# Kernel optimization log

Hardware: AMD Instinct MI355X
Metric: run time of the kernel (lower is better)

Reference implementation:

```python
import jax, jax.numpy as jnp
import numpy as np

N_NODES = 50000
E_EDGES = 800000
NODE_DIM = 64
HID = 128


def _leaky(x):
    return jnp.where(x > 0, x, 0.2 * x)


def _gat_conv(x, W, a_src, a_dst, b, src, dst, heads, out_ch, concat):
    # x: [N, in]; W: [in, heads*out]; a_src/a_dst: [heads, out]
    N = x.shape[0]
    h = (x @ W).reshape(N, heads, out_ch)            # [N, H, C]
    s = (h * a_src[None]).sum(-1)                    # [N, H]
    d = (h * a_dst[None]).sum(-1)                    # [N, H]
    e = _leaky(s[src] + d[dst])                      # [E, H]
    m = jax.ops.segment_max(e, dst, num_segments=N)  # segment softmax (stable)
    ex = jnp.exp(e - m[dst])
    denom = jax.ops.segment_sum(ex, dst, num_segments=N)
    alpha = ex / denom[dst]                          # [E, H] (self-loops -> denom>0)
    out = jax.ops.segment_sum(h[src] * alpha[..., None], dst, num_segments=N)
    out = out.reshape(N, heads * out_ch) if concat else out.mean(axis=1)
    return out + b


def setup_inputs() -> dict:
    key = jax.random.key(0)
    ks = jax.random.split(key, 16)
    sc = 0.1
    inp = {
        "x": jax.random.normal(ks[0], (N_NODES, NODE_DIM), jnp.float32),
        "edge_index": jax.random.randint(ks[1], (2, E_EDGES), 0, N_NODES, jnp.int64),
        "fc_w": jax.random.normal(ks[2], (NODE_DIM, HID), jnp.float32) * sc,
        "fc_b": jnp.zeros((HID,), jnp.float32),
        "W1": jax.random.normal(ks[3], (HID, 2 * HID), jnp.float32) * sc,
        "asrc1": jax.random.normal(ks[4], (2, HID), jnp.float32) * sc,
        "adst1": jax.random.normal(ks[5], (2, HID), jnp.float32) * sc,
        "b1": jnp.zeros((2 * HID,), jnp.float32),
        "Wm": jax.random.normal(ks[6], (4, 2 * HID, 2 * HID), jnp.float32) * sc,
        "asrcm": jax.random.normal(ks[7], (4, 2, HID), jnp.float32) * sc,
        "adstm": jax.random.normal(ks[8], (4, 2, HID), jnp.float32) * sc,
        "bm": jnp.zeros((4, 2 * HID), jnp.float32),
        "W6": jax.random.normal(ks[9], (2 * HID, HID), jnp.float32) * sc,
        "asrc6": jax.random.normal(ks[10], (1, HID), jnp.float32) * sc,
        "adst6": jax.random.normal(ks[11], (1, HID), jnp.float32) * sc,
        "b6": jnp.zeros((HID,), jnp.float32),
    }
    return inp


def reference(x, edge_index, fc_w, fc_b, W1, asrc1, adst1, b1,
              Wm, asrcm, adstm, bm, W6, asrc6, adst6, b6):
    N = x.shape[0]
    loops = jnp.arange(N, dtype=edge_index.dtype)
    src = jnp.concatenate([edge_index[0], loops])  # add_self_loops=True (PyG default)
    dst = jnp.concatenate([edge_index[1], loops])

    out = jax.nn.relu(x @ fc_w + fc_b)
    out = _gat_conv(out, W1, asrc1, adst1, b1, src, dst, 2, HID, True)
    for i in range(4):
        out = _gat_conv(out, Wm[i], asrcm[i], adstm[i], bm[i], src, dst, 2, HID, True)
    out = _gat_conv(out, W6, asrc6, adst6, b6, src, dst, 1, HID, True)
    return out
```

## Files before the change

kernel.cpp:

```cpp
#include <hip/hip_runtime.h>
#include <cstdint>
#include <cstddef>

#define NN 50000
#define EE 800000
#define ET 850000

typedef unsigned short ushort_t;
typedef unsigned int uint_t;
using frag_ab = __attribute__((ext_vector_type(8))) short;
using f32x4   = __attribute__((ext_vector_type(4))) float;

__device__ inline ushort_t f2b(float x) {
  union { float f; unsigned int u; } c; c.f = x;
  unsigned int u = c.u;
  u += 0x7fffu + ((u >> 16) & 1u);
  return (ushort_t)(u >> 16);
}
__device__ inline float b2f(uint_t u) {
  union { unsigned int u; float f; } c; c.u = u << 16;
  return c.f;
}

__device__ inline void gload16(const ushort_t* g, ushort_t* l) {
  __builtin_amdgcn_global_load_lds(
      (const __attribute__((address_space(1))) unsigned int*)g,
      (__attribute__((address_space(3))) unsigned int*)l, 16, 0, 0);
}

__global__ __launch_bounds__(256) void k_count(const int* __restrict__ edge,
                                               int* __restrict__ counts) {
  int e = blockIdx.x * 256 + threadIdx.x;
  if (e >= ET) return;
  int dd = (e < EE) ? edge[EE + e] : (e - EE);
  atomicAdd(&counts[dd], 1);
}

__global__ __launch_bounds__(1024) void k_scan1(const int* __restrict__ counts,
                                                int* __restrict__ scn,
                                                int* __restrict__ bsum) {
  __shared__ int tmp[1024];
  int tid = threadIdx.x;
  int idx = blockIdx.x * 1024 + tid;
  int v = (idx < NN) ? counts[idx] : 0;
  tmp[tid] = v;
  __syncthreads();
  for (int o = 1; o < 1024; o <<= 1) {
    int u = (tid >= o) ? tmp[tid - o] : 0;
    __syncthreads();
    tmp[tid] += u;
    __syncthreads();
  }
  if (idx < NN) scn[idx] = tmp[tid] - v;
  if (tid == 1023) bsum[blockIdx.x] = tmp[1023];
}

__global__ __launch_bounds__(64) void k_scan2(const int* __restrict__ bsum,
                                              int* __restrict__ boff) {
  int l = threadIdx.x;
  const int NB = (NN + 1023) / 1024;
  int v = (l < NB) ? bsum[l] : 0;
  int own = v;
  for (int o = 1; o < 64; o <<= 1) {
    int u = __shfl_up(v, o);
    if (l >= o) v += u;
  }
  if (l < NB) boff[l] = v - own;
}

__global__ __launch_bounds__(1024) void k_scan3(const int* __restrict__ scn,
                                                const int* __restrict__ boff,
                                                int* __restrict__ row_ptr,
                                                int* __restrict__ cursor) {
  int idx = blockIdx.x * 1024 + threadIdx.x;
  if (idx < NN) {
    int v = scn[idx] + boff[blockIdx.x];
    row_ptr[idx] = v;
    cursor[idx] = v;
  }
  if (idx == 0) row_ptr[NN] = ET;
}

__global__ __launch_bounds__(256) void k_fill(const int* __restrict__ edge,
                                              int* __restrict__ cursor,
                                              int* __restrict__ col_src) {
  int e = blockIdx.x * 256 + threadIdx.x;
  if (e >= ET) return;
  int ss, dd;
  if (e < EE) { ss = edge[e]; dd = edge[EE + e]; }
  else        { ss = dd = e - EE; }
  int pos = atomicAdd(&cursor[dd], 1);
  col_src[pos] = ss;
}

__global__ __launch_bounds__(256) void k_prep_w(const float* __restrict__ fc_w,
                                                const float* __restrict__ W1,
                                                const float* __restrict__ Wm,
                                                const float* __restrict__ W6,
                                                ushort_t* __restrict__ fcWt,
                                                ushort_t* __restrict__ W1t,
                                                ushort_t* __restrict__ Wmt,
                                                ushort_t* __restrict__ W6t) {
  int i = blockIdx.x * 256 + threadIdx.x;
  if (i < 128 * 64) { int n = i >> 6, k = i & 63; fcWt[i] = f2b(fc_w[k * 128 + n]); return; }
  i -= 128 * 64;
  if (i < 256 * 128) { int n = i >> 7, k = i & 127; W1t[i] = f2b(W1[k * 256 + n]); return; }
  i -= 256 * 128;
  if (i < 4 * 256 * 256) {
    int l = i >> 16, r2 = i & 65535, n = r2 >> 8, k = r2 & 255;
    Wmt[i] = f2b(Wm[(size_t)l * 65536 + k * 256 + n]); return;
  }
  i -= 4 * 256 * 256;
  if (i < 128 * 256) { int n = i >> 8, k = i & 255; W6t[i] = f2b(W6[k * 128 + n]); return; }
}

__global__ __launch_bounds__(256) void k_gemm_f32(const float* __restrict__ A,
                                                  const ushort_t* __restrict__ Bt,
                                                  ushort_t* __restrict__ C,
                                                  int M, int K, int Nc,
                                                  const float* __restrict__ bias) {
  __shared__ ushort_t As[128 * 40];
  __shared__ ushort_t Bs[128 * 40];
  int row0 = blockIdx.x * 128;
  int col0 = blockIdx.y * 128;
  int t = threadIdx.x;
  int lane = t & 63, w = t >> 6;
  int wr = w >> 1, wc = w & 1;
  int r = lane & 15, kg = lane >> 4;

  f32x4 acc[4][4];
#pragma unroll
  for (int m = 0; m < 4; ++m)
#pragma unroll
    for (int n = 0; n < 4; ++n) acc[m][n] = (f32x4){0.f, 0.f, 0.f, 0.f};

  for (int k0 = 0; k0 < K; k0 += 32) {
    __syncthreads();
#pragma unroll
    for (int rep = 0; rep < 4; ++rep) {
      int c = t + rep * 256;
      int row = c >> 3, kc = c & 7;
      int grow = row0 + row;
      if (grow < M) {
        float4 v = *(const float4*)&A[(size_t)grow * K + k0 + kc * 4];
        ushort4 u;
        u.x = f2b(v.x); u.y = f2b(v.y); u.z = f2b(v.z); u.w = f2b(v.w);
        *(ushort4*)&As[row * 40 + kc * 4] = u;
      }
    }
#pragma unroll
    for (int rep = 0; rep < 2; ++rep) {
      int c = t + rep * 256;
      int row = c >> 2, kc = c & 3;
      uint4 v = *(const uint4*)&Bt[(size_t)(col0 + row) * K + k0 + kc * 8];
      *(uint4*)&Bs[row * 40 + kc * 8] = v;
    }
    __syncthreads();

    frag_ab a[4], b[4];
#pragma unroll
    for (int m = 0; m < 4; ++m)
      a[m] = *(const frag_ab*)&As[(wr * 64 + m * 16 + r) * 40 + kg * 8];
#pragma unroll
    for (int n = 0; n < 4; ++n)
      b[n] = *(const frag_ab*)&Bs[(wc * 64 + n * 16 + r) * 40 + kg * 8];
#pragma unroll
    for (int m = 0; m < 4; ++m)
#pragma unroll
      for (int n = 0; n < 4; ++n)
        acc[m][n] = __builtin_amdgcn_mfma_f32_16x16x32_bf16(a[m], b[n], acc[m][n], 0, 0, 0);
  }

#pragma unroll
  for (int m = 0; m < 4; ++m) {
    int gr0 = row0 + wr * 64 + m * 16 + kg * 4;
#pragma unroll
    for (int q = 0; q < 4; ++q) {
      int grow = gr0 + q;
      if (grow >= M) continue;
#pragma unroll
      for (int n = 0; n < 4; ++n) {
        int gcol = col0 + wc * 64 + n * 16 + r;
        float val = acc[m][n][q] + bias[gcol];
        val = fmaxf(val, 0.f);
        C[(size_t)grow * Nc + gcol] = f2b(val);
      }
    }
  }
}

__global__ __launch_bounds__(256) void k_gemm64(const ushort_t* __restrict__ A,
                                                const ushort_t* __restrict__ Bt,
                                                ushort_t* __restrict__ C,
                                                int M, int K, int Nc,
                                                const float* __restrict__ a_src,
                                                const float* __restrict__ a_dst,
                                                float* __restrict__ sbuf,
                                                float* __restrict__ dbuf,
                                                int H) {
  __shared__ ushort_t As[128 * 64];
  __shared__ ushort_t Bs[128 * 64];
  __shared__ float sdred[128][2][2];
  int row0 = blockIdx.x * 128;
  int col0 = blockIdx.y * 128;
  int t = threadIdx.x;
  int lane = t & 63, w = t >> 6;
  int wr = w >> 1, wc = w & 1;
  int r = lane & 15, kg = lane >> 4;

  f32x4 acc[4][4];
#pragma unroll
  for (int m = 0; m < 4; ++m)
#pragma unroll
    for (int n = 0; n < 4; ++n) acc[m][n] = (f32x4){0.f, 0.f, 0.f, 0.f};

  for (int k0 = 0; k0 < K; k0 += 64) {
    __syncthreads();
#pragma unroll
    for (int i = 0; i < 4; ++i) {
      int c = w * 4 + i;
      int b = c * 1024 + lane * 16;
      int row = b >> 7;
      int ks = ((b >> 4) & 7) ^ (row & 7);
      const ushort_t* ga = A + (size_t)(row0 + row) * K + k0 + ks * 8;
      if (row0 + row < M) gload16(ga, &As[c * 512]);
      const ushort_t* gb = Bt + (size_t)(col0 + row) * K + k0 + ks * 8;
      gload16(gb, &Bs[c * 512]);
    }
    __syncthreads();

#pragma unroll
    for (int kk = 0; kk < 2; ++kk) {
      frag_ab af[4], bf[4];
#pragma unroll
      for (int m = 0; m < 4; ++m) {
        int row = wr * 64 + m * 16 + r;
        int byte = row * 128 + ((kk * 64 + kg * 16) ^ ((row & 7) << 4));
        af[m] = *(const frag_ab*)((const char*)As + byte);
      }
#pragma unroll
      for (int n = 0; n < 4; ++n) {
        int row = wc * 64 + n * 16 + r;
        int byte = row * 128 + ((kk * 64 + kg * 16) ^ ((row & 7) << 4));
        bf[n] = *(const frag_ab*)((const char*)Bs + byte);
      }
#pragma unroll
      for (int m = 0; m < 4; ++m)
#pragma unroll
        for (int n = 0; n < 4; ++n)
          acc[m][n] = __builtin_amdgcn_mfma_f32_16x16x32_bf16(af[m], bf[n], acc[m][n], 0, 0, 0);
    }
  }

  int head = blockIdx.y;
  float as_[4], ad_[4];
#pragma unroll
  for (int n = 0; n < 4; ++n) {
    int cloc = wc * 64 + n * 16 + r;
    as_[n] = a_src[head * 128 + cloc];
    ad_[n] = a_dst[head * 128 + cloc];
  }

#pragma unroll
  for (int m = 0; m < 4; ++m) {
    int gr0 = row0 + wr * 64 + m * 16 + kg * 4;
#pragma unroll
    for (int q = 0; q < 4; ++q) {
      int grow = gr0 + q;
      float ps = 0.f, pd = 0.f;
      if (grow < M) {
#pragma unroll
        for (int n = 0; n < 4; ++n) {
          int gcol = col0 + wc * 64 + n * 16 + r;
          float val = acc[m][n][q];
          ps += val * as_[n]; pd += val * ad_[n];
          C[(size_t)grow * Nc + gcol] = f2b(val);
        }
      }
#pragma unroll
      for (int o = 1; o < 16; o <<= 1) {
        ps += __shfl_xor(ps, o);
        pd += __shfl_xor(pd, o);
      }
      int row_loc = wr * 64 + m * 16 + kg * 4 + q;
      if (r == 0) { sdred[row_loc][wc][0] = ps; sdred[row_loc][wc][1] = pd; }
    }
  }
  __syncthreads();
  int row = t >> 1, which = t & 1;
  int grow = row0 + row;
  if (grow < M) {
    float v = sdred[row][0][which] + sdred[row][1][which];
    float* dst = which ? dbuf : sbuf;
    dst[(size_t)grow * H + head] = v;
  }
}

__global__ __launch_bounds__(256) void k_agg2(const ushort_t* __restrict__ h2,
                                              const float* __restrict__ s,
                                              const float* __restrict__ dv,
                                              const int* __restrict__ row_ptr,
                                              const int* __restrict__ col_src,
                                              const float* __restrict__ bias,
                                              uint4* __restrict__ out) {
  int wid = threadIdx.x >> 6, l = threadIdx.x & 63;
  int n = blockIdx.x * 4 + wid;
  if (n >= NN) return;
  int beg = row_ptr[n], end = row_ptr[n + 1];
  float2 tdn = ((const float2*)dv)[n];
  float dn0 = tdn.x, dn1 = tdn.y;

  float m0 = -1e30f, d0 = 0.f, m1 = -1e30f, d1 = 0.f;
  for (int e = beg + l; e < end; e += 64) {
    int src = col_src[e];
    float2 sv = ((const float2*)s)[src];
    float x0 = sv.x + dn0; x0 = x0 > 0.f ? x0 : 0.2f * x0;
    if (x0 > m0) { d0 = d0 * __expf(m0 - x0) + 1.f; m0 = x0; } else d0 += __expf(x0 - m0);
    float x1 = sv.y + dn1; x1 = x1 > 0.f ? x1 : 0.2f * x1;
    if (x1 > m1) { d1 = d1 * __expf(m1 - x1) + 1.f; m1 = x1; } else d1 += __expf(x1 - m1);
  }
#pragma unroll
  for (int o = 1; o < 64; o <<= 1) {
    float mo = __shfl_xor(m0, o), dno = __shfl_xor(d0, o);
    float M2 = fmaxf(m0, mo);
    d0 = d0 * __expf(m0 - M2) + dno * __expf(mo - M2);
    m0 = M2;
    mo = __shfl_xor(m1, o); dno = __shfl_xor(d1, o);
    M2 = fmaxf(m1, mo);
    d1 = d1 * __expf(m1 - M2) + dno * __expf(mo - M2);
    m1 = M2;
  }

  int hw = l >> 5, lh = l & 31;
  int hd = lh >> 4;
  const uint4* hrow = (const uint4*)h2;
  float a0 = 0.f, a1 = 0.f, a2 = 0.f, a3 = 0.f;
  float a4 = 0.f, a5 = 0.f, a6 = 0.f, a7 = 0.f;

  for (int c = beg; c < end; c += 32) {
    int cnt = min(32, end - c);
    float alpv = 0.f; int srcv = 0;
    if (l < 2 * cnt) {
      int e = c + (l >> 1), hi = l & 1;
      srcv = col_src[e];
      float x = s[srcv * 2 + hi] + (hi ? dn1 : dn0);
      x = x > 0.f ? x : 0.2f * x;
      alpv = __expf(x - (hi ? m1 : m0));
    }
    int e = 0;
    for (; e + 4 <= cnt + 1; e += 4) {
      int ep0 = e + hw, ep1 = e + 2 + hw;
      int s0 = __shfl(srcv, 2 * ep0);
      int s1 = __shfl(srcv, 2 * ep1);
      float p0 = __shfl(alpv, 2 * ep0 + hd);
      float p1 = __shfl(alpv, 2 * ep1 + hd);
      if (ep0 >= cnt) p0 = 0.f;
      if (ep1 >= cnt) p1 = 0.f;
      uint4 v0 = hrow[(size_t)s0 * 32 + lh];
      uint4 v1 = hrow[(size_t)s1 * 32 + lh];
      a0 = fmaf(p0, b2f(v0.x & 0xffffu), a0); a1 = fmaf(p0, b2f(v0.x >> 16), a1);
      a2 = fmaf(p0, b2f(v0.y & 0xffffu), a2); a3 = fmaf(p0, b2f(v0.y >> 16), a3);
      a4 = fmaf(p0, b2f(v0.z & 0xffffu), a4); a5 = fmaf(p0, b2f(v0.z >> 16), a5);
      a6 = fmaf(p0, b2f(v0.w & 0xffffu), a6); a7 = fmaf(p0, b2f(v0.w >> 16), a7);
      a0 = fmaf(p1, b2f(v1.x & 0xffffu), a0); a1 = fmaf(p1, b2f(v1.x >> 16), a1);
      a2 = fmaf(p1, b2f(v1.y & 0xffffu), a2); a3 = fmaf(p1, b2f(v1.y >> 16), a3);
      a4 = fmaf(p1, b2f(v1.z & 0xffffu), a4); a5 = fmaf(p1, b2f(v1.z >> 16), a5);
      a6 = fmaf(p1, b2f(v1.w & 0xffffu), a6); a7 = fmaf(p1, b2f(v1.w >> 16), a7);
    }
    for (; e < cnt; e += 2) {
      int ep = e + hw;
      int s0 = __shfl(srcv, 2 * ep);
      float p = __shfl(alpv, 2 * ep + hd);
      if (ep >= cnt) p = 0.f;
      uint4 v = hrow[(size_t)s0 * 32 + lh];
      a0 = fmaf(p, b2f(v.x & 0xffffu), a0); a1 = fmaf(p, b2f(v.x >> 16), a1);
      a2 = fmaf(p, b2f(v.y & 0xffffu), a2); a3 = fmaf(p, b2f(v.y >> 16), a3);
      a4 = fmaf(p, b2f(v.z & 0xffffu), a4); a5 = fmaf(p, b2f(v.z >> 16), a5);
      a6 = fmaf(p, b2f(v.w & 0xffffu), a6); a7 = fmaf(p, b2f(v.w >> 16), a7);
    }
  }
  a0 += __shfl_xor(a0, 32); a1 += __shfl_xor(a1, 32);
  a2 += __shfl_xor(a2, 32); a3 += __shfl_xor(a3, 32);
  a4 += __shfl_xor(a4, 32); a5 += __shfl_xor(a5, 32);
  a6 += __shfl_xor(a6, 32); a7 += __shfl_xor(a7, 32);

  if (hw == 0) {
    float dh = hd ? d1 : d0;
    float inv = 1.f / dh;
    float4 b0 = ((const float4*)bias)[2 * lh];
    float4 b1 = ((const float4*)bias)[2 * lh + 1];
    uint4 ov;
    ov.x = (uint_t)f2b(a0 * inv + b0.x) | ((uint_t)f2b(a1 * inv + b0.y) << 16);
    ov.y = (uint_t)f2b(a2 * inv + b0.z) | ((uint_t)f2b(a3 * inv + b0.w) << 16);
    ov.z = (uint_t)f2b(a4 * inv + b1.x) | ((uint_t)f2b(a5 * inv + b1.y) << 16);
    ov.w = (uint_t)f2b(a6 * inv + b1.z) | ((uint_t)f2b(a7 * inv + b1.w) << 16);
    out[(size_t)n * 32 + lh] = ov;
  }
}

__global__ __launch_bounds__(256) void k_agg1(const ushort_t* __restrict__ h2,
                                              const float* __restrict__ s,
                                              const float* __restrict__ dv,
                                              const int* __restrict__ row_ptr,
                                              const int* __restrict__ col_src,
                                              const float* __restrict__ bias,
                                              float* __restrict__ out) {
  int wid = threadIdx.x >> 6, l = threadIdx.x & 63;
  int n = blockIdx.x * 4 + wid;
  if (n >= NN) return;
  int beg = row_ptr[n], end = row_ptr[n + 1];
  float dn0 = dv[n];

  float m0 = -1e30f, d0 = 0.f;
  for (int e = beg + l; e < end; e += 64) {
    float x0 = s[col_src[e]] + dn0;
    x0 = x0 > 0.f ? x0 : 0.2f * x0;
    if (x0 > m0) { d0 = d0 * __expf(m0 - x0) + 1.f; m0 = x0; } else d0 += __expf(x0 - m0);
  }
#pragma unroll
  for (int o = 1; o < 64; o <<= 1) {
    float mo = __shfl_xor(m0, o), dno = __shfl_xor(d0, o);
    float M2 = fmaxf(m0, mo);
    d0 = d0 * __expf(m0 - M2) + dno * __expf(mo - M2);
    m0 = M2;
  }

  int hw = l >> 4, lh = l & 15;
  const uint4* hrow = (const uint4*)h2;
  float a0 = 0.f, a1 = 0.f, a2 = 0.f, a3 = 0.f;
  float a4 = 0.f, a5 = 0.f, a6 = 0.f, a7 = 0.f;

  for (int c = beg; c < end; c += 64) {
    int cnt = min(64, end - c);
    float alpv = 0.f; int srcv = 0;
    if (l < cnt) {
      srcv = col_src[c + l];
      float x = s[srcv] + dn0;
      x = x > 0.f ? x : 0.2f * x;
      alpv = __expf(x - m0);
    }
    for (int e = 0; e < cnt; e += 4) {
      int ep = e + hw;
      int s0 = __shfl(srcv, ep);
      float p = __shfl(alpv, ep);
      if (ep >= cnt) p = 0.f;
      uint4 v = hrow[(size_t)s0 * 16 + lh];
      a0 = fmaf(p, b2f(v.x & 0xffffu), a0); a1 = fmaf(p, b2f(v.x >> 16), a1);
      a2 = fmaf(p, b2f(v.y & 0xffffu), a2); a3 = fmaf(p, b2f(v.y >> 16), a3);
      a4 = fmaf(p, b2f(v.z & 0xffffu), a4); a5 = fmaf(p, b2f(v.z >> 16), a5);
      a6 = fmaf(p, b2f(v.w & 0xffffu), a6); a7 = fmaf(p, b2f(v.w >> 16), a7);
    }
  }
#pragma unroll
  for (int o = 16; o < 64; o <<= 1) {
    a0 += __shfl_xor(a0, o); a1 += __shfl_xor(a1, o);
    a2 += __shfl_xor(a2, o); a3 += __shfl_xor(a3, o);
    a4 += __shfl_xor(a4, o); a5 += __shfl_xor(a5, o);
    a6 += __shfl_xor(a6, o); a7 += __shfl_xor(a7, o);
  }
  if (hw == 0) {
    float inv = 1.f / d0;
    float4 b0 = ((const float4*)bias)[2 * lh];
    float4 b1 = ((const float4*)bias)[2 * lh + 1];
    float4 o0 = make_float4(a0 * inv + b0.x, a1 * inv + b0.y, a2 * inv + b0.z, a3 * inv + b0.w);
    float4 o1 = make_float4(a4 * inv + b1.x, a5 * inv + b1.y, a6 * inv + b1.z, a7 * inv + b1.w);
    ((float4*)out)[(size_t)n * 32 + 2 * lh] = o0;
    ((float4*)out)[(size_t)n * 32 + 2 * lh + 1] = o1;
  }
}

extern "C" void kernel_launch(void* const* d_in, const int* in_sizes, int n_in,
                              void* d_out, int out_size, void* d_ws, size_t ws_size,
                              hipStream_t stream) {
  const float* x     = (const float*)d_in[0];
  const int*   edge  = (const int*)d_in[1];
  const float* fc_w  = (const float*)d_in[2];
  const float* fc_b  = (const float*)d_in[3];
  const float* W1    = (const float*)d_in[4];
  const float* asrc1 = (const float*)d_in[5];
  const float* adst1 = (const float*)d_in[6];
  const float* b1    = (const float*)d_in[7];
  const float* Wm    = (const float*)d_in[8];
  const float* asrcm = (const float*)d_in[9];
  const float* adstm = (const float*)d_in[10];
  const float* bm    = (const float*)d_in[11];
  const float* W6    = (const float*)d_in[12];
  const float* asrc6 = (const float*)d_in[13];
  const float* adst6 = (const float*)d_in[14];
  const float* b6    = (const float*)d_in[15];

  char* w = (char*)d_ws;
  size_t off = 0;
  auto carve = [&](size_t bytes) -> char* {
    char* p = w + off;
    off = (off + bytes + 255) & ~(size_t)255;
    return p;
  };
  ushort_t* feat0 = (ushort_t*)carve((size_t)NN * 256 * 2);
  ushort_t* feat1 = (ushort_t*)carve((size_t)NN * 256 * 2);
  ushort_t* hbuf  = (ushort_t*)carve((size_t)NN * 256 * 2);
  float* sbuf   = (float*)carve((size_t)NN * 2 * 4);
  float* dbuf   = (float*)carve((size_t)NN * 2 * 4);
  ushort_t* fcWt = (ushort_t*)carve((size_t)128 * 64 * 2);
  ushort_t* W1t  = (ushort_t*)carve((size_t)256 * 128 * 2);
  ushort_t* Wmt  = (ushort_t*)carve((size_t)4 * 256 * 256 * 2);
  ushort_t* W6t  = (ushort_t*)carve((size_t)128 * 256 * 2);
  int* counts   = (int*)carve((size_t)NN * 4);
  int* row_ptr  = (int*)carve((size_t)(NN + 1) * 4);
  int* cursor   = (int*)carve((size_t)NN * 4);
  int* col_src  = (int*)carve((size_t)ET * 4);
  int* scn      = (int*)carve((size_t)NN * 4);
  int* bsum     = (int*)carve((size_t)64 * 4);
  int* boff     = (int*)carve((size_t)64 * 4);
  (void)ws_size;

  k_prep_w<<<(335872 + 255) / 256, 256, 0, stream>>>(fc_w, W1, Wm, W6, fcWt, W1t, Wmt, W6t);

  hipMemsetAsync(counts, 0, (size_t)NN * 4, stream);
  int eb = (ET + 255) / 256;
  const int NB = (NN + 1023) / 1024;
  k_count<<<eb, 256, 0, stream>>>(edge, counts);
  k_scan1<<<NB, 1024, 0, stream>>>(counts, scn, bsum);
  k_scan2<<<1, 64, 0, stream>>>(bsum, boff);
  k_scan3<<<NB, 1024, 0, stream>>>(scn, boff, row_ptr, cursor);
  k_fill<<<eb, 256, 0, stream>>>(edge, cursor, col_src);

  dim3 g1((NN + 127) / 128, 1), g2((NN + 127) / 128, 2);
  int ab = (NN + 3) / 4;

  auto gat = [&](const ushort_t* in, int K, const ushort_t* Wt, const float* a_s,
                 const float* a_d, const float* bias, void* outp, int H) {
    k_gemm64<<<(H == 2 ? g2 : g1), 256, 0, stream>>>(
        in, Wt, hbuf, NN, K, H * 128, a_s, a_d, sbuf, dbuf, H);
    if (H == 2)
      k_agg2<<<ab, 256, 0, stream>>>(hbuf, sbuf, dbuf, row_ptr, col_src, bias, (uint4*)outp);
    else
      k_agg1<<<ab, 256, 0, stream>>>(hbuf, sbuf, dbuf, row_ptr, col_src, bias, (float*)outp);
  };

  k_gemm_f32<<<g1, 256, 0, stream>>>(x, fcWt, feat0, NN, 64, 128, fc_b);

  gat(feat0, 128, W1t, asrc1, adst1, b1, feat1, 2);

  const ushort_t* cur = feat1;
  ushort_t* nxt = feat0;
  for (int i = 0; i < 4; ++i) {
    gat(cur, 256, Wmt + (size_t)i * 256 * 256, asrcm + (size_t)i * 2 * 128,
        adstm + (size_t)i * 2 * 128, bm + (size_t)i * 256, nxt, 2);
    const ushort_t* tmp = cur;
    cur = nxt;
    nxt = (ushort_t*)tmp;
  }

  gat(cur, 256, W6t, asrc6, adst6, b6, d_out, 1);
}
```

Before: 599.3 us.

## Add single-pass low-degree path and packed FMA to GAT aggregation kernels

Both aggregation kernels gain a fast path for nodes with degree at most 64. In that path each lane loads its edge's source and score once, and plain max and sum wave reductions replace the online-softmax loop and the second reload of col_src and s. The accumulation now uses packed two-wide FMA on unpacked bf16 pairs with precomputed byte offsets and a fixed unrolled inner loop. Padding lanes carry zero probability instead of a per-edge bound check, and the general path is kept for high-degree nodes.

```diff
diff --git a/kernel.cpp b/kernel.cpp
--- a/kernel.cpp
+++ b/kernel.cpp
@@ -10,6 +10,7 @@
 typedef unsigned int uint_t;
 using frag_ab = __attribute__((ext_vector_type(8))) short;
 using f32x4   = __attribute__((ext_vector_type(4))) float;
+using f32x2   = __attribute__((ext_vector_type(2))) float;
 
 __device__ inline ushort_t f2b(float x) {
   union { float f; unsigned int u; } c; c.f = x;
@@ -20,6 +21,11 @@
 __device__ inline float b2f(uint_t u) {
   union { unsigned int u; float f; } c; c.u = u << 16;
   return c.f;
+}
+__device__ inline f32x2 unp2(uint_t u) {
+  union { uint_t u; float f; } lo, hi;
+  lo.u = u << 16; hi.u = u & 0xffff0000u;
+  f32x2 r; r.x = lo.f; r.y = hi.f; return r;
 }
 
 __device__ inline void gload16(const ushort_t* g, ushort_t* l) {
@@ -307,82 +313,109 @@
   int n = blockIdx.x * 4 + wid;
   if (n >= NN) return;
   int beg = row_ptr[n], end = row_ptr[n + 1];
+  int deg = end - beg;
   float2 tdn = ((const float2*)dv)[n];
   float dn0 = tdn.x, dn1 = tdn.y;
-
-  float m0 = -1e30f, d0 = 0.f, m1 = -1e30f, d1 = 0.f;
-  for (int e = beg + l; e < end; e += 64) {
-    int src = col_src[e];
-    float2 sv = ((const float2*)s)[src];
-    float x0 = sv.x + dn0; x0 = x0 > 0.f ? x0 : 0.2f * x0;
-    if (x0 > m0) { d0 = d0 * __expf(m0 - x0) + 1.f; m0 = x0; } else d0 += __expf(x0 - m0);
-    float x1 = sv.y + dn1; x1 = x1 > 0.f ? x1 : 0.2f * x1;
-    if (x1 > m1) { d1 = d1 * __expf(m1 - x1) + 1.f; m1 = x1; } else d1 += __expf(x1 - m1);
-  }
-#pragma unroll
-  for (int o = 1; o < 64; o <<= 1) {
-    float mo = __shfl_xor(m0, o), dno = __shfl_xor(d0, o);
-    float M2 = fmaxf(m0, mo);
-    d0 = d0 * __expf(m0 - M2) + dno * __expf(mo - M2);
-    m0 = M2;
-    mo = __shfl_xor(m1, o); dno = __shfl_xor(d1, o);
-    M2 = fmaxf(m1, mo);
-    d1 = d1 * __expf(m1 - M2) + dno * __expf(mo - M2);
-    m1 = M2;
-  }
-
-  int hw = l >> 5, lh = l & 31;
-  int hd = lh >> 4;
-  const uint4* hrow = (const uint4*)h2;
-  float a0 = 0.f, a1 = 0.f, a2 = 0.f, a3 = 0.f;
-  float a4 = 0.f, a5 = 0.f, a6 = 0.f, a7 = 0.f;
-
-  for (int c = beg; c < end; c += 32) {
-    int cnt = min(32, end - c);
-    float alpv = 0.f; int srcv = 0;
-    if (l < 2 * cnt) {
-      int e = c + (l >> 1), hi = l & 1;
-      srcv = col_src[e];
-      float x = s[srcv * 2 + hi] + (hi ? dn1 : dn0);
-      x = x > 0.f ? x : 0.2f * x;
-      alpv = __expf(x - (hi ? m1 : m0));
-    }
-    int e = 0;
-    for (; e + 4 <= cnt + 1; e += 4) {
-      int ep0 = e + hw, ep1 = e + 2 + hw;
-      int s0 = __shfl(srcv, 2 * ep0);
-      int s1 = __shfl(srcv, 2 * ep1);
-      float p0 = __shfl(alpv, 2 * ep0 + hd);
-      float p1 = __shfl(alpv, 2 * ep1 + hd);
-      if (ep0 >= cnt) p0 = 0.f;
-      if (ep1 >= cnt) p1 = 0.f;
-      uint4 v0 = hrow[(size_t)s0 * 32 + lh];
-      uint4 v1 = hrow[(size_t)s1 * 32 + lh];
-      a0 = fmaf(p0, b2f(v0.x & 0xffffu), a0); a1 = fmaf(p0, b2f(v0.x >> 16), a1);
-      a2 = fmaf(p0, b2f(v0.y & 0xffffu), a2); a3 = fmaf(p0, b2f(v0.y >> 16), a3);
-      a4 = fmaf(p0, b2f(v0.z & 0xffffu), a4); a5 = fmaf(p0, b2f(v0.z >> 16), a5);
-      a6 = fmaf(p0, b2f(v0.w & 0xffffu), a6); a7 = fmaf(p0, b2f(v0.w >> 16), a7);
-      a0 = fmaf(p1, b2f(v1.x & 0xffffu), a0); a1 = fmaf(p1, b2f(v1.x >> 16), a1);
-      a2 = fmaf(p1, b2f(v1.y & 0xffffu), a2); a3 = fmaf(p1, b2f(v1.y >> 16), a3);
-      a4 = fmaf(p1, b2f(v1.z & 0xffffu), a4); a5 = fmaf(p1, b2f(v1.z >> 16), a5);
-      a6 = fmaf(p1, b2f(v1.w & 0xffffu), a6); a7 = fmaf(p1, b2f(v1.w >> 16), a7);
-    }
-    for (; e < cnt; e += 2) {
-      int ep = e + hw;
-      int s0 = __shfl(srcv, 2 * ep);
-      float p = __shfl(alpv, 2 * ep + hd);
-      if (ep >= cnt) p = 0.f;
-      uint4 v = hrow[(size_t)s0 * 32 + lh];
-      a0 = fmaf(p, b2f(v.x & 0xffffu), a0); a1 = fmaf(p, b2f(v.x >> 16), a1);
-      a2 = fmaf(p, b2f(v.y & 0xffffu), a2); a3 = fmaf(p, b2f(v.y >> 16), a3);
-      a4 = fmaf(p, b2f(v.z & 0xffffu), a4); a5 = fmaf(p, b2f(v.z >> 16), a5);
-      a6 = fmaf(p, b2f(v.w & 0xffffu), a6); a7 = fmaf(p, b2f(v.w >> 16), a7);
-    }
-  }
-  a0 += __shfl_xor(a0, 32); a1 += __shfl_xor(a1, 32);
-  a2 += __shfl_xor(a2, 32); a3 += __shfl_xor(a3, 32);
-  a4 += __shfl_xor(a4, 32); a5 += __shfl_xor(a5, 32);
-  a6 += __shfl_xor(a6, 32); a7 += __shfl_xor(a7, 32);
+  int hw = l >> 5, lh = l & 31, hd = lh >> 4;
+  const char* hb = (const char*)h2 + lh * 16;
+
+  f32x2 A0 = {0.f, 0.f}, A1 = {0.f, 0.f}, A2 = {0.f, 0.f}, A3 = {0.f, 0.f};
+  float d0, d1;
+
+  if (deg <= 64) {
+    int srcv = 0; float x0 = -1e30f, x1 = -1e30f;
+    if (l < deg) {
+      srcv = col_src[beg + l];
+      float2 sv = ((const float2*)s)[srcv];
+      x0 = sv.x + dn0; x0 = x0 > 0.f ? x0 : 0.2f * x0;
+      x1 = sv.y + dn1; x1 = x1 > 0.f ? x1 : 0.2f * x1;
+    }
+    float m0 = x0, m1 = x1;
+#pragma unroll
+    for (int o = 1; o < 64; o <<= 1) {
+      m0 = fmaxf(m0, __shfl_xor(m0, o));
+      m1 = fmaxf(m1, __shfl_xor(m1, o));
+    }
+    float p0 = __expf(x0 - m0), p1 = __expf(x1 - m1);
+    d0 = p0; d1 = p1;
+#pragma unroll
+    for (int o = 1; o < 64; o <<= 1) {
+      d0 += __shfl_xor(d0, o);
+      d1 += __shfl_xor(d1, o);
+    }
+    int offv = srcv << 9;
+    for (int e = 0; e < deg; e += 8) {
+#pragma unroll
+      for (int i = 0; i < 4; ++i) {
+        int ep = e + 2 * i + hw;
+        int off = __shfl(offv, ep);
+        float pa0 = __shfl(p0, ep);
+        float pa1 = __shfl(p1, ep);
+        float pa = hd ? pa1 : pa0;
+        uint4 v = *(const uint4*)(hb + off);
+        f32x2 pp = {pa, pa};
+        A0 = __builtin_elementwise_fma(unp2(v.x), pp, A0);
+        A1 = __builtin_elementwise_fma(unp2(v.y), pp, A1);
+        A2 = __builtin_elementwise_fma(unp2(v.z), pp, A2);
+        A3 = __builtin_elementwise_fma(unp2(v.w), pp, A3);
+      }
+    }
+  } else {
+    float m0 = -1e30f, m1 = -1e30f;
+    d0 = 0.f; d1 = 0.f;
+    for (int e = beg + l; e < end; e += 64) {
+      int src = col_src[e];
+      float2 sv = ((const float2*)s)[src];
+      float x0 = sv.x + dn0; x0 = x0 > 0.f ? x0 : 0.2f * x0;
+      if (x0 > m0) { d0 = d0 * __expf(m0 - x0) + 1.f; m0 = x0; } else d0 += __expf(x0 - m0);
+      float x1 = sv.y + dn1; x1 = x1 > 0.f ? x1 : 0.2f * x1;
+      if (x1 > m1) { d1 = d1 * __expf(m1 - x1) + 1.f; m1 = x1; } else d1 += __expf(x1 - m1);
+    }
+#pragma unroll
+    for (int o = 1; o < 64; o <<= 1) {
+      float mo = __shfl_xor(m0, o), dno = __shfl_xor(d0, o);
+      float M2 = fmaxf(m0, mo);
+      d0 = d0 * __expf(m0 - M2) + dno * __expf(mo - M2);
+      m0 = M2;
+      mo = __shfl_xor(m1, o); dno = __shfl_xor(d1, o);
+      M2 = fmaxf(m1, mo);
+      d1 = d1 * __expf(m1 - M2) + dno * __expf(mo - M2);
+      m1 = M2;
+    }
+    for (int c = beg; c < end; c += 64) {
+      int cnt = min(64, end - c);
+      int srcv = 0; float x0 = -1e30f, x1 = -1e30f;
+      if (l < cnt) {
+        srcv = col_src[c + l];
+        float2 sv = ((const float2*)s)[srcv];
+        x0 = sv.x + dn0; x0 = x0 > 0.f ? x0 : 0.2f * x0;
+        x1 = sv.y + dn1; x1 = x1 > 0.f ? x1 : 0.2f * x1;
+      }
+      float p0 = __expf(x0 - m0), p1 = __expf(x1 - m1);
+      int offv = srcv << 9;
+      for (int e = 0; e < cnt; e += 8) {
+#pragma unroll
+        for (int i = 0; i < 4; ++i) {
+          int ep = e + 2 * i + hw;
+          int off = __shfl(offv, ep);
+          float pa0 = __shfl(p0, ep);
+          float pa1 = __shfl(p1, ep);
+          float pa = hd ? pa1 : pa0;
+          uint4 v = *(const uint4*)(hb + off);
+          f32x2 pp = {pa, pa};
+          A0 = __builtin_elementwise_fma(unp2(v.x), pp, A0);
+          A1 = __builtin_elementwise_fma(unp2(v.y), pp, A1);
+          A2 = __builtin_elementwise_fma(unp2(v.z), pp, A2);
+          A3 = __builtin_elementwise_fma(unp2(v.w), pp, A3);
+        }
+      }
+    }
+  }
+
+  A0.x += __shfl_xor(A0.x, 32); A0.y += __shfl_xor(A0.y, 32);
+  A1.x += __shfl_xor(A1.x, 32); A1.y += __shfl_xor(A1.y, 32);
+  A2.x += __shfl_xor(A2.x, 32); A2.y += __shfl_xor(A2.y, 32);
+  A3.x += __shfl_xor(A3.x, 32); A3.y += __shfl_xor(A3.y, 32);
 
   if (hw == 0) {
     float dh = hd ? d1 : d0;
@@ -390,10 +423,10 @@
     float4 b0 = ((const float4*)bias)[2 * lh];
     float4 b1 = ((const float4*)bias)[2 * lh + 1];
     uint4 ov;
-    ov.x = (uint_t)f2b(a0 * inv + b0.x) | ((uint_t)f2b(a1 * inv + b0.y) << 16);
-    ov.y = (uint_t)f2b(a2 * inv + b0.z) | ((uint_t)f2b(a3 * inv + b0.w) << 16);
-    ov.z = (uint_t)f2b(a4 * inv + b1.x) | ((uint_t)f2b(a5 * inv + b1.y) << 16);
-    ov.w = (uint_t)f2b(a6 * inv + b1.z) | ((uint_t)f2b(a7 * inv + b1.w) << 16);
+    ov.x = (uint_t)f2b(A0.x * inv + b0.x) | ((uint_t)f2b(A0.y * inv + b0.y) << 16);
+    ov.y = (uint_t)f2b(A1.x * inv + b0.z) | ((uint_t)f2b(A1.y * inv + b0.w) << 16);
+    ov.z = (uint_t)f2b(A2.x * inv + b1.x) | ((uint_t)f2b(A2.y * inv + b1.y) << 16);
+    ov.w = (uint_t)f2b(A3.x * inv + b1.z) | ((uint_t)f2b(A3.y * inv + b1.w) << 16);
     out[(size_t)n * 32 + lh] = ov;
   }
 }
@@ -409,61 +442,98 @@
   int n = blockIdx.x * 4 + wid;
   if (n >= NN) return;
   int beg = row_ptr[n], end = row_ptr[n + 1];
+  int deg = end - beg;
   float dn0 = dv[n];
-
-  float m0 = -1e30f, d0 = 0.f;
-  for (int e = beg + l; e < end; e += 64) {
-    float x0 = s[col_src[e]] + dn0;
-    x0 = x0 > 0.f ? x0 : 0.2f * x0;
-    if (x0 > m0) { d0 = d0 * __expf(m0 - x0) + 1.f; m0 = x0; } else d0 += __expf(x0 - m0);
-  }
-#pragma unroll
-  for (int o = 1; o < 64; o <<= 1) {
-    float mo = __shfl_xor(m0, o), dno = __shfl_xor(d0, o);
-    float M2 = fmaxf(m0, mo);
-    d0 = d0 * __expf(m0 - M2) + dno * __expf(mo - M2);
-    m0 = M2;
-  }
-
   int hw = l >> 4, lh = l & 15;
-  const uint4* hrow = (const uint4*)h2;
-  float a0 = 0.f, a1 = 0.f, a2 = 0.f, a3 = 0.f;
-  float a4 = 0.f, a5 = 0.f, a6 = 0.f, a7 = 0.f;
-
-  for (int c = beg; c < end; c += 64) {
-    int cnt = min(64, end - c);
-    float alpv = 0.f; int srcv = 0;
-    if (l < cnt) {
-      srcv = col_src[c + l];
-      float x = s[srcv] + dn0;
-      x = x > 0.f ? x : 0.2f * x;
-      alpv = __expf(x - m0);
-    }
-    for (int e = 0; e < cnt; e += 4) {
-      int ep = e + hw;
-      int s0 = __shfl(srcv, ep);
-      float p = __shfl(alpv, ep);
-      if (ep >= cnt) p = 0.f;
-      uint4 v = hrow[(size_t)s0 * 16 + lh];
-      a0 = fmaf(p, b2f(v.x & 0xffffu), a0); a1 = fmaf(p, b2f(v.x >> 16), a1);
-      a2 = fmaf(p, b2f(v.y & 0xffffu), a2); a3 = fmaf(p, b2f(v.y >> 16), a3);
-      a4 = fmaf(p, b2f(v.z & 0xffffu), a4); a5 = fmaf(p, b2f(v.z >> 16), a5);
-      a6 = fmaf(p, b2f(v.w & 0xffffu), a6); a7 = fmaf(p, b2f(v.w >> 16), a7);
-    }
-  }
+  const char* hb = (const char*)h2 + lh * 16;
+
+  f32x2 A0 = {0.f, 0.f}, A1 = {0.f, 0.f}, A2 = {0.f, 0.f}, A3 = {0.f, 0.f};
+  float d0;
+
+  if (deg <= 64) {
+    int srcv = 0; float x0 = -1e30f;
+    if (l < deg) {
+      srcv = col_src[beg + l];
+      x0 = s[srcv] + dn0; x0 = x0 > 0.f ? x0 : 0.2f * x0;
+    }
+    float m0 = x0;
+#pragma unroll
+    for (int o = 1; o < 64; o <<= 1) m0 = fmaxf(m0, __shfl_xor(m0, o));
+    float p0 = __expf(x0 - m0);
+    d0 = p0;
+#pragma unroll
+    for (int o = 1; o < 64; o <<= 1) d0 += __shfl_xor(d0, o);
+    int offv = srcv << 8;
+    for (int e = 0; e < deg; e += 8) {
+#pragma unroll
+      for (int i = 0; i < 2; ++i) {
+        int ep = e + 4 * i + hw;
+        int off = __shfl(offv, ep);
+        float pa = __shfl(p0, ep);
+        uint4 v = *(const uint4*)(hb + off);
+        f32x2 pp = {pa, pa};
+        A0 = __builtin_elementwise_fma(unp2(v.x), pp, A0);
+        A1 = __builtin_elementwise_fma(unp2(v.y), pp, A1);
+        A2 = __builtin_elementwise_fma(unp2(v.z), pp, A2);
+        A3 = __builtin_elementwise_fma(unp2(v.w), pp, A3);
+      }
+    }
+  } else {
+    float m0 = -1e30f;
+    d0 = 0.f;
+    for (int e = beg + l; e < end; e += 64) {
+      float x0 = s[col_src[e]] + dn0;
+      x0 = x0 > 0.f ? x0 : 0.2f * x0;
+      if (x0 > m0) { d0 = d0 * __expf(m0 - x0) + 1.f; m0 = x0; } else d0 += __expf(x0 - m0);
+    }
+#pragma unroll
+    for (int o = 1; o < 64; o <<= 1) {
+      float mo = __shfl_xor(m0, o), dno = __shfl_xor(d0, o);
+      float M2 = fmaxf(m0, mo);
+      d0 = d0 * __expf(m0 - M2) + dno * __expf(mo - M2);
+      m0 = M2;
+    }
+    for (int c = beg; c < end; c += 64) {
+      int cnt = min(64, end - c);
+      int srcv = 0; float x0 = -1e30f;
+      if (l < cnt) {
+        srcv = col_src[c + l];
+        x0 = s[srcv] + dn0; x0 = x0 > 0.f ? x0 : 0.2f * x0;
+      }
+      float p0 = __expf(x0 - m0);
+      int offv = srcv << 8;
+      for (int e = 0; e < cnt; e += 8) {
+#pragma unroll
+        for (int i = 0; i < 2; ++i) {
+          int ep = e + 4 * i + hw;
+          int off = __shfl(offv, ep);
+          float pa = __shfl(p0, ep);
+          uint4 v = *(const uint4*)(hb + off);
+          f32x2 pp = {pa, pa};
+          A0 = __builtin_elementwise_fma(unp2(v.x), pp, A0);
+          A1 = __builtin_elementwise_fma(unp2(v.y), pp, A1);
+          A2 = __builtin_elementwise_fma(unp2(v.z), pp, A2);
+          A3 = __builtin_elementwise_fma(unp2(v.w), pp, A3);
+        }
+      }
+    }
+  }
+
 #pragma unroll
   for (int o = 16; o < 64; o <<= 1) {
-    a0 += __shfl_xor(a0, o); a1 += __shfl_xor(a1, o);
-    a2 += __shfl_xor(a2, o); a3 += __shfl_xor(a3, o);
-    a4 += __shfl_xor(a4, o); a5 += __shfl_xor(a5, o);
-    a6 += __shfl_xor(a6, o); a7 += __shfl_xor(a7, o);
+    A0.x += __shfl_xor(A0.x, o); A0.y += __shfl_xor(A0.y, o);
+    A1.x += __shfl_xor(A1.x, o); A1.y += __shfl_xor(A1.y, o);
+    A2.x += __shfl_xor(A2.x, o); A2.y += __shfl_xor(A2.y, o);
+    A3.x += __shfl_xor(A3.x, o); A3.y += __shfl_xor(A3.y, o);
   }
   if (hw == 0) {
     float inv = 1.f / d0;
     float4 b0 = ((const float4*)bias)[2 * lh];
     float4 b1 = ((const float4*)bias)[2 * lh + 1];
-    float4 o0 = make_float4(a0 * inv + b0.x, a1 * inv + b0.y, a2 * inv + b0.z, a3 * inv + b0.w);
-    float4 o1 = make_float4(a4 * inv + b1.x, a5 * inv + b1.y, a6 * inv + b1.z, a7 * inv + b1.w);
+    float4 o0 = make_float4(A0.x * inv + b0.x, A0.y * inv + b0.y,
+                            A1.x * inv + b0.z, A1.y * inv + b0.w);
+    float4 o1 = make_float4(A2.x * inv + b1.x, A2.y * inv + b1.y,
+                            A3.x * inv + b1.z, A3.y * inv + b1.w);
     ((float4*)out)[(size_t)n * 32 + 2 * lh] = o0;
     ((float4*)out)[(size_t)n * 32 + 2 * lh + 1] = o1;
   }
```

Result: no change. 599.7 us (+0.1%).
